# Kernel optimization log

Measured on AMD Instinct MI355X. Metric: run time of the kernel, lower is better.

## Reference

```python
import jax, jax.numpy as jnp
import numpy as np

B, T = 32, 1000
NN, NB, CTX = 512, 16, 64
EMB = 256
DCAT = 3 * EMB
H, L = 256, 4
PN, PB = 512, 2
S, V = 8, 64


def setup_inputs() -> dict:
    key = jax.random.key(0)
    ks = jax.random.split(key, 20)
    r = lambda i, shape, sc=1.0: jax.random.normal(ks[i], shape, dtype=jnp.float32) * sc
    nu_log = jnp.log(-jnp.log(jax.random.uniform(ks[8], (L, H), minval=0.5, maxval=0.95)))
    inp = {
        'neural_input': r(0, (B, T, NN)),
        'behavior_input': r(1, (B, T, NB)),
        'session_id': jax.random.randint(ks[2], (B,), 0, V),
        'subject_id': jax.random.randint(ks[3], (B,), 0, S),
        'session_table': r(4, (V, CTX), 0.02),
        'neural_W': r(5, (S, EMB, NN), 1.0 / np.sqrt(NN)),
        'neural_b': jnp.zeros((S, EMB), jnp.float32),
        'behavior_W': r(6, (S, EMB, NB), 1.0 / np.sqrt(NB)),
        'behavior_b': jnp.zeros((S, EMB), jnp.float32),
        'ctx_W': r(7, (EMB, CTX), 1.0 / np.sqrt(CTX)),
        'ctx_b': jnp.zeros((EMB,), jnp.float32),
        'nu_log': nu_log,
        'theta_log': jnp.log(jax.random.uniform(ks[9], (L, H), minval=1e-4, maxval=6.283)),
        'gamma_log': 0.5 * jnp.log1p(-jnp.exp(-2.0 * jnp.exp(nu_log))),
        'B_re': r(10, (L, H, DCAT), 1.0 / np.sqrt(2 * DCAT)),
        'B_im': r(11, (L, H, DCAT), 1.0 / np.sqrt(2 * DCAT)),
        'C_re': r(12, (L, DCAT, H), 1.0 / np.sqrt(H)),
        'C_im': r(13, (L, DCAT, H), 1.0 / np.sqrt(H)),
        'D_skip': r(14, (L, DCAT)),
        'dec_n_W': r(15, (S, PN, DCAT), 1.0 / np.sqrt(DCAT)),
        'dec_n_b': jnp.zeros((S, PN), jnp.float32),
        'dec_b_W': r(16, (S, PB, DCAT), 1.0 / np.sqrt(DCAT)),
        'dec_b_b': jnp.zeros((S, PB), jnp.float32),
    }
    return inp


def _lru(u, nu_log, theta_log, gamma_log, B_re, B_im, C_re, C_im, D_skip):
    # Linear Recurrent Unit: complex diagonal recurrence x_t = lam*x_{t-1} + gamma*B u_t
    lam = jnp.exp(-jnp.exp(nu_log) + 1j * jnp.exp(theta_log))  # [H]
    g = jnp.exp(gamma_log)[:, None]
    Bu = (jnp.einsum('bti,hi->bth', u, B_re * g)
          + 1j * jnp.einsum('bti,hi->bth', u, B_im * g))  # [B,T,H] complex

    def step(x, bu_t):
        x = lam * x + bu_t
        return x, x

    x0 = jnp.zeros((u.shape[0], nu_log.shape[0]), jnp.complex64)
    _, xs = jax.lax.scan(step, x0, jnp.swapaxes(Bu, 0, 1))
    xs = jnp.swapaxes(xs, 0, 1)  # [B,T,H]
    y = jnp.einsum('bth,oh->bto', xs, C_re + 1j * C_im).real + D_skip * u
    return y


def _forward(neural_input, behavior_input, session_table, neural_W, neural_b,
             behavior_W, behavior_b, ctx_W, ctx_b, nu_log, theta_log, gamma_log,
             B_re, B_im, C_re, C_im, D_skip, dec_n_W, dec_n_b, dec_b_W, dec_b_b,
             session_id, subject_id):
    act = jax.nn.relu
    Bsz, Ts, _ = neural_input.shape
    # session-token embedding -> context embedder (Linear is per-timestep, so embed once then broadcast)
    ctx = act(session_table[session_id] @ ctx_W.T + ctx_b)  # [B,EMB]
    ctx = jnp.broadcast_to(ctx[:, None, :], (Bsz, Ts, ctx.shape[-1]))
    # subject-routed embedders: gather per-sample weights, one batched GEMM
    en = act(jnp.einsum('btf,bef->bte', neural_input, neural_W[subject_id])
             + neural_b[subject_id][:, None, :])
    eb = act(jnp.einsum('btf,bef->bte', behavior_input, behavior_W[subject_id])
             + behavior_b[subject_id][:, None, :])
    h = jnp.concatenate([en, eb, ctx], axis=-1)  # [B,T,3*EMB]
    for l in range(nu_log.shape[0]):
        h = _lru(h, nu_log[l], theta_log[l], gamma_log[l],
                 B_re[l], B_im[l], C_re[l], C_im[l], D_skip[l])
    # subject-routed decoders
    pred_n = jax.nn.softplus(jnp.einsum('btd,bod->bto', h, dec_n_W[subject_id])
                             + dec_n_b[subject_id][:, None, :])
    pred_b = (jnp.einsum('btd,bod->bto', h, dec_b_W[subject_id])
              + dec_b_b[subject_id][:, None, :])
    return pred_n, pred_b


def reference(neural_input, behavior_input, session_id, subject_id, session_table,
              neural_W, neural_b, behavior_W, behavior_b, ctx_W, ctx_b,
              nu_log, theta_log, gamma_log, B_re, B_im, C_re, C_im, D_skip,
              dec_n_W, dec_n_b, dec_b_W, dec_b_b):
    return _forward(neural_input, behavior_input, session_table, neural_W, neural_b,
                    behavior_W, behavior_b, ctx_W, ctx_b, nu_log, theta_log, gamma_log,
                    B_re, B_im, C_re, C_im, D_skip, dec_n_W, dec_n_b, dec_b_W, dec_b_b,
                    session_id, subject_id)
```

## Files before the change

kernel.cpp:

```cpp
#include <hip/hip_runtime.h>

typedef __bf16 bf16;
typedef __bf16 bf16x8 __attribute__((ext_vector_type(8)));
typedef float f32x4 __attribute__((ext_vector_type(4)));

#define AS1 __attribute__((address_space(1)))
#define AS3 __attribute__((address_space(3)))

__device__ __forceinline__ void gll16(const void* g, void* l) {
    __builtin_amdgcn_global_load_lds((const AS1 void*)g, (AS3 void*)l, 16, 0, 0);
}

template<int EPI>
__device__ __forceinline__
void gemm_body(const bf16* __restrict__ Abase, long long aBstride, int lda,
               const bf16* __restrict__ Wbase, long long wSstride,
               const float* __restrict__ biasBase, int biasStride,
               void* __restrict__ Cbase, long long cBstride, int ldc,
               const float* __restrict__ dskip,
               const bf16* __restrict__ Ubase, long long uBstride,
               const int* __restrict__ subj,
               int M, int K, int nbn, char* smem)
{
    const int tid = threadIdx.x;
    const int lane = tid & 63;
    const int wid = tid >> 6;
    const int wm = wid >> 1, wn = wid & 1;
    const int l15 = lane & 15, lhi = lane >> 4;
    const int sw7 = l15 & 7;

    const int nwg = gridDim.x;
    const int bid = blockIdx.x;
    const int q = nwg >> 3, r = nwg & 7;
    const int xcd = bid & 7;
    const int sw = xcd * q + (xcd < r ? xcd : r) + (bid >> 3);
    const int m0 = (sw / nbn) * 256;
    const int n0 = (sw % nbn) * 128;

    const int b = blockIdx.z;
    const int s = subj ? subj[b] : 0;
    const bf16* A = Abase + (size_t)b * aBstride;
    const bf16* W = Wbase + (size_t)s * wSstride;
    const float* bias = biasBase ? biasBase + (size_t)s * biasStride : nullptr;
    const bf16* U = Ubase ? Ubase + (size_t)b * uBstride : nullptr;
    const size_t coff = (size_t)b * cBstride;
    const int Mc = M - 1;

    f32x4 acc[4][4];
    #pragma unroll
    for (int i = 0; i < 4; ++i)
        #pragma unroll
        for (int j = 0; j < 4; ++j)
            acc[i][j] = f32x4{0.f, 0.f, 0.f, 0.f};

    int rA[4], rB[4];
    #pragma unroll
    for (int f = 0; f < 4; ++f) {
        rA[f] = (wm*64 + f*16 + l15) * 128;
        rB[f] = (wn*64 + f*16 + l15) * 128;
    }

    const int sub  = tid >> 3;
    const int slot = tid & 7;
    const int ldsw = (wid << 10);

    auto stage = [&](int kt, int bufo) {
        #pragma unroll
        for (int c = 0; c < 4; ++c) {
            const int row = c*64 + sub;
            const int gk = (kt << 6) + ((slot ^ (row & 7)) << 3);
            int ar = m0 + row; if (ar > Mc) ar = Mc;
            gll16(A + (size_t)ar * lda + gk, smem + bufo + c*8192 + ldsw);
        }
        #pragma unroll
        for (int c = 0; c < 2; ++c) {
            const int row = c*64 + sub;
            const int gk = (kt << 6) + ((slot ^ (row & 7)) << 3);
            gll16(W + (size_t)(n0 + row) * K + gk, smem + bufo + 32768 + c*8192 + ldsw);
        }
    };

    const int nkt = K >> 6;
    stage(0, 0);
    if (nkt > 1) stage(1, 49152);
    asm volatile("s_waitcnt vmcnt(6)" ::: "memory");
    __builtin_amdgcn_s_barrier();

    int curo = 0, nno = 98304;
    for (int t = 0; t < nkt; ++t) {
        if (t + 2 < nkt) stage(t + 2, nno);

        const char* cb = smem + curo;
        #pragma unroll
        for (int kk = 0; kk < 2; ++kk) {
            const int so_ = (((kk << 2) | lhi) ^ sw7) << 4;
            bf16x8 af[4], bg[4];
            #pragma unroll
            for (int f = 0; f < 4; ++f) af[f] = *(const bf16x8*)(cb + rA[f] + so_);
            #pragma unroll
            for (int g = 0; g < 4; ++g) bg[g] = *(const bf16x8*)(cb + 32768 + rB[g] + so_);
            #pragma unroll
            for (int i = 0; i < 4; ++i)
                #pragma unroll
                for (int j = 0; j < 4; ++j)
                    acc[i][j] = __builtin_amdgcn_mfma_f32_16x16x32_bf16(
                        af[i], bg[j], acc[i][j], 0, 0, 0);
        }

        if (t + 2 < nkt) {
            asm volatile("s_waitcnt vmcnt(6)" ::: "memory");
        } else if (t + 1 < nkt) {
            asm volatile("s_waitcnt vmcnt(0)" ::: "memory");
        }
        if (t + 1 < nkt) __builtin_amdgcn_s_barrier();

        curo = (curo == 98304) ? 0 : curo + 49152;
        nno  = (nno  == 98304) ? 0 : nno  + 49152;
    }

    __syncthreads();
    #pragma unroll
    for (int i = 0; i < 4; ++i) {
        #pragma unroll
        for (int j = 0; j < 4; ++j) {
            const int colb = (wn*64 + j*16 + l15) * 2;
            const f32x4 v = acc[i][j];
            #pragma unroll
            for (int qq = 0; qq < 4; ++qq) {
                const int row = wm*64 + i*16 + lhi*4 + qq;
                const int ad = row*256 + (colb & 15) + ((((colb >> 4) ^ (row & 7)) & 15) << 4);
                *(bf16*)(smem + ad) = (bf16)v[qq];
            }
        }
    }
    __syncthreads();

    #pragma unroll
    for (int u = 0; u < 8; ++u) {
        const int chunk = u*512 + tid;
        const int rr = chunk >> 4, ss = chunk & 15;
        const int gr = m0 + rr;
        if (gr >= M) continue;
        const int col = n0 + ss*8;
        const bf16x8 v = *(const bf16x8*)(smem + rr*256 + ((ss ^ (rr & 7)) << 4));
        if constexpr (EPI == 0) {
            const size_t ci = coff + (size_t)gr * ldc + col;
            *(bf16x8*)((bf16*)Cbase + ci) = v;
        } else if constexpr (EPI == 1) {
            const float4 b0 = *(const float4*)(bias + col);
            const float4 b1 = *(const float4*)(bias + col + 4);
            bf16x8 o;
            o[0] = (bf16)fmaxf((float)v[0] + b0.x, 0.f);
            o[1] = (bf16)fmaxf((float)v[1] + b0.y, 0.f);
            o[2] = (bf16)fmaxf((float)v[2] + b0.z, 0.f);
            o[3] = (bf16)fmaxf((float)v[3] + b0.w, 0.f);
            o[4] = (bf16)fmaxf((float)v[4] + b1.x, 0.f);
            o[5] = (bf16)fmaxf((float)v[5] + b1.y, 0.f);
            o[6] = (bf16)fmaxf((float)v[6] + b1.z, 0.f);
            o[7] = (bf16)fmaxf((float)v[7] + b1.w, 0.f);
            const size_t ci = coff + (size_t)gr * ldc + col;
            *(bf16x8*)((bf16*)Cbase + ci) = o;
        } else if constexpr (EPI == 2) {
            const bf16x8 uv = *(const bf16x8*)(U + (size_t)gr * ldc + col);
            const float4 d0 = *(const float4*)(dskip + col);
            const float4 d1 = *(const float4*)(dskip + col + 4);
            bf16x8 o;
            o[0] = (bf16)((float)v[0] + d0.x * (float)uv[0]);
            o[1] = (bf16)((float)v[1] + d0.y * (float)uv[1]);
            o[2] = (bf16)((float)v[2] + d0.z * (float)uv[2]);
            o[3] = (bf16)((float)v[3] + d0.w * (float)uv[3]);
            o[4] = (bf16)((float)v[4] + d1.x * (float)uv[4]);
            o[5] = (bf16)((float)v[5] + d1.y * (float)uv[5]);
            o[6] = (bf16)((float)v[6] + d1.z * (float)uv[6]);
            o[7] = (bf16)((float)v[7] + d1.w * (float)uv[7]);
            const size_t ci = coff + (size_t)gr * ldc + col;
            *(bf16x8*)((bf16*)Cbase + ci) = o;
        } else {
            const float4 b0 = *(const float4*)(bias + col);
            const float4 b1 = *(const float4*)(bias + col + 4);
            float xv[8];
            xv[0] = (float)v[0] + b0.x; xv[1] = (float)v[1] + b0.y;
            xv[2] = (float)v[2] + b0.z; xv[3] = (float)v[3] + b0.w;
            xv[4] = (float)v[4] + b1.x; xv[5] = (float)v[5] + b1.y;
            xv[6] = (float)v[6] + b1.z; xv[7] = (float)v[7] + b1.w;
            float4 o0, o1;
            #pragma unroll
            for (int e = 0; e < 8; ++e) {
                const float x = xv[e];
                const float sp = fmaxf(x, 0.f) + log1pf(expf(-fabsf(x)));
                if (e < 4) ((float*)&o0)[e] = sp; else ((float*)&o1)[e-4] = sp;
            }
            const size_t ci = coff + (size_t)gr * ldc + col;
            *(float4*)((float*)Cbase + ci) = o0;
            *(float4*)((float*)Cbase + ci + 4) = o1;
        }
    }
}

#define GEMM_WRAP(NAME, EPI)                                                     \
__global__ __launch_bounds__(512, 2)                                             \
void NAME(const bf16* __restrict__ Abase, long long aBstride, int lda,           \
          const bf16* __restrict__ Wbase, long long wSstride,                    \
          const float* __restrict__ biasBase, int biasStride,                    \
          void* __restrict__ Cbase, long long cBstride, int ldc,                 \
          const float* __restrict__ dskip,                                       \
          const bf16* __restrict__ Ubase, long long uBstride,                    \
          const int* __restrict__ subj, int M, int K, int nbn)                   \
{                                                                                \
    __shared__ char smem[147456];                                                \
    gemm_body<EPI>(Abase, aBstride, lda, Wbase, wSstride, biasBase, biasStride,  \
                   Cbase, cBstride, ldc, dskip, Ubase, uBstride, subj,           \
                   M, K, nbn, smem);                                             \
}
GEMM_WRAP(gemm_en,  1)
GEMM_WRAP(gemm_bu,  0)
GEMM_WRAP(gemm_y,   2)
GEMM_WRAP(gemm_dec, 3)

__global__ void scan_finals(const bf16* __restrict__ Bu,
                            const float* __restrict__ nu_log,
                            const float* __restrict__ theta_log,
                            float2* __restrict__ finals)
{
    const int g = blockIdx.x * 256 + threadIdx.x;
    const int h = g & 255;
    const int c = (g >> 8) % 40;
    const int b = g / 10240;
    const float a  = expf(nu_log[h]);
    const float th = expf(theta_log[h]);
    const float mag = expf(-a);
    const float lre = mag * cosf(th), lim = mag * sinf(th);
    float xre = 0.f, xim = 0.f;
    const bf16* p = Bu + ((size_t)(b*1000 + c*25)) * 512 + h;
    for (int i = 0; i < 25; ++i) {
        const float bre = (float)p[0], bim = (float)p[256];
        const float nre = lre*xre - lim*xim + bre;
        const float nim = lre*xim + lim*xre + bim;
        xre = nre; xim = nim;
        p += 512;
    }
    finals[(b*40 + c)*256 + h] = make_float2(xre, xim);
}

__global__ void scan_carry(const float2* __restrict__ finals,
                           float2* __restrict__ carry,
                           const float* __restrict__ nu_log,
                           const float* __restrict__ theta_log)
{
    const int g = blockIdx.x * 256 + threadIdx.x;
    const int h = g & 255;
    const int b = g >> 8;
    const float a  = expf(nu_log[h]);
    const float th = expf(theta_log[h]);
    const float mag = expf(-25.f * a);
    const float ang = 25.f * th;
    const float cre = mag * cosf(ang), cim = mag * sinf(ang);
    float pre = 0.f, pim = 0.f;
    for (int c = 0; c < 40; ++c) {
        const int idx = (b*40 + c)*256 + h;
        carry[idx] = make_float2(pre, pim);
        const float2 f = finals[idx];
        const float nre = f.x + cre*pre - cim*pim;
        const float nim = f.y + cre*pim + cim*pre;
        pre = nre; pim = nim;
    }
}

__global__ void scan_emit(const bf16* __restrict__ Bu,
                          const float2* __restrict__ carry,
                          const float* __restrict__ nu_log,
                          const float* __restrict__ theta_log,
                          bf16* __restrict__ xs)
{
    const int g = blockIdx.x * 256 + threadIdx.x;
    const int h = g & 255;
    const int c = (g >> 8) % 40;
    const int b = g / 10240;
    const float a  = expf(nu_log[h]);
    const float th = expf(theta_log[h]);
    const float mag = expf(-a);
    const float lre = mag * cosf(th), lim = mag * sinf(th);
    const float2 cr = carry[(b*40 + c)*256 + h];
    float xre = cr.x, xim = cr.y;
    const bf16* p = Bu + ((size_t)(b*1000 + c*25)) * 512 + h;
    bf16* qp = xs + ((size_t)(b*1000 + c*25)) * 512 + h;
    for (int i = 0; i < 25; ++i) {
        const float bre = (float)p[0], bim = (float)p[256];
        const float nre = lre*xre - lim*xim + bre;
        const float nim = lre*xim + lim*xre + bim;
        xre = nre; xim = nim;
        qp[0] = (bf16)xre; qp[256] = (bf16)xim;
        p += 512; qp += 512;
    }
}

__global__ void cast8_kern(const float* __restrict__ src, bf16* __restrict__ dst, int n8)
{
    const int i = blockIdx.x * 256 + threadIdx.x;
    if (i >= n8) return;
    const float4* s = (const float4*)src + (size_t)i*2;
    const float4 v0 = s[0], v1 = s[1];
    bf16x8 o;
    o[0] = (bf16)v0.x; o[1] = (bf16)v0.y; o[2] = (bf16)v0.z; o[3] = (bf16)v0.w;
    o[4] = (bf16)v1.x; o[5] = (bf16)v1.y; o[6] = (bf16)v1.z; o[7] = (bf16)v1.w;
    *((bf16x8*)dst + i) = o;
}

__global__ void packWB_kern(const float* __restrict__ Bre, const float* __restrict__ Bim,
                            const float* __restrict__ glog, bf16* __restrict__ WB)
{
    const int idx = blockIdx.x * 256 + threadIdx.x;
    if (idx >= 4*512*768) return;
    const int l = idx / (512*768);
    const int r = idx - l*(512*768);
    const int n = r / 768;
    const int k = r - n*768;
    float v;
    if (n < 256) v = Bre[((size_t)(l*256 + n))*768 + k] * expf(glog[l*256 + n]);
    else         v = Bim[((size_t)(l*256 + (n-256)))*768 + k] * expf(glog[l*256 + (n-256)]);
    WB[idx] = (bf16)v;
}

__global__ void packWC_kern(const float* __restrict__ Cre, const float* __restrict__ Cim,
                            bf16* __restrict__ WC)
{
    const int idx = blockIdx.x * 256 + threadIdx.x;
    if (idx >= 4*768*512) return;
    const int l = idx / (768*512);
    const int r = idx - l*(768*512);
    const int o = r / 512;
    const int k = r - o*512;
    const float v = (k < 256) ? Cre[((size_t)(l*768 + o))*256 + k]
                              : -Cim[((size_t)(l*768 + o))*256 + (k - 256)];
    WC[idx] = (bf16)v;
}

__global__ void ctx_kern(const float* __restrict__ st, const int* __restrict__ sess,
                         const float* __restrict__ cW, const float* __restrict__ cb,
                         float* __restrict__ ctx)
{
    const int b = blockIdx.x;
    const int e = threadIdx.x;
    const int sid = sess[b];
    const float* r = st + (size_t)sid * 64;
    const float* w = cW + (size_t)e * 64;
    float acc = cb[e];
    #pragma unroll 8
    for (int i = 0; i < 64; ++i) acc += r[i] * w[i];
    ctx[b*256 + e] = fmaxf(acc, 0.f);
}

__global__ void ebctx_kern(const float* __restrict__ behav,
                           const float* __restrict__ bW,
                           const float* __restrict__ bB,
                           const int* __restrict__ subj,
                           const float* __restrict__ ctx,
                           bf16* __restrict__ h0)
{
    const int b  = blockIdx.x >> 3;
    const int tc = blockIdx.x & 7;
    const int e = threadIdx.x;
    const int s = subj[b];
    float wreg[16];
    const float* w = bW + ((size_t)(s*256) + e)*16;
    #pragma unroll
    for (int i = 0; i < 16; ++i) wreg[i] = w[i];
    const float bb_ = bB[s*256 + e];
    const bf16 cx = (bf16)ctx[b*256 + e];
    const int t0 = tc * 125;
    for (int t = t0; t < t0 + 125; ++t) {
        const int blk = b*1000 + t;
        const float* bi = behav + (size_t)blk * 16;
        float acc = bb_;
        #pragma unroll
        for (int i = 0; i < 16; ++i) acc += bi[i] * wreg[i];
        bf16* hp = h0 + (size_t)blk * 768;
        hp[256 + e] = (bf16)fmaxf(acc, 0.f);
        hp[512 + e] = cx;
    }
}

__global__ void predb_kern(const bf16* __restrict__ h, const float* __restrict__ W,
                           const float* __restrict__ bb, const int* __restrict__ subj,
                           float* __restrict__ out)
{
    const int lane = threadIdx.x & 63;
    const int wid  = threadIdx.x >> 6;
    const int row  = blockIdx.x * 4 + wid;
    const int b = row / 1000;
    const int s = subj[b];
    const bf16* hr = h + (size_t)row * 768;
    const float* w0 = W + (size_t)(s*2) * 768;
    const float* w1 = w0 + 768;
    float a0 = 0.f, a1 = 0.f;
    #pragma unroll
    for (int j = 0; j < 12; ++j) {
        const int idx = j*64 + lane;
        const float hv = (float)hr[idx];
        a0 += hv * w0[idx];
        a1 += hv * w1[idx];
    }
    #pragma unroll
    for (int m = 32; m >= 1; m >>= 1) {
        a0 += __shfl_xor(a0, m);
        a1 += __shfl_xor(a1, m);
    }
    if (lane == 0) {
        out[(size_t)row*2 + 0] = a0 + bb[s*2 + 0];
        out[(size_t)row*2 + 1] = a1 + bb[s*2 + 1];
    }
}

extern "C" void kernel_launch(void* const* d_in, const int* in_sizes, int n_in,
                              void* d_out, int out_size, void* d_ws, size_t ws_size,
                              hipStream_t stream)
{
    const float* neural_input   = (const float*)d_in[0];
    const float* behavior_input = (const float*)d_in[1];
    const int*   session_id     = (const int*)d_in[2];
    const int*   subject_id     = (const int*)d_in[3];
    const float* session_table  = (const float*)d_in[4];
    const float* neural_W  = (const float*)d_in[5];
    const float* neural_b  = (const float*)d_in[6];
    const float* behavior_W = (const float*)d_in[7];
    const float* behavior_b = (const float*)d_in[8];
    const float* ctx_W = (const float*)d_in[9];
    const float* ctx_b = (const float*)d_in[10];
    const float* nu_log    = (const float*)d_in[11];
    const float* theta_log = (const float*)d_in[12];
    const float* gamma_log = (const float*)d_in[13];
    const float* B_re = (const float*)d_in[14];
    const float* B_im = (const float*)d_in[15];
    const float* C_re = (const float*)d_in[16];
    const float* C_im = (const float*)d_in[17];
    const float* D_skip = (const float*)d_in[18];
    const float* dec_n_W = (const float*)d_in[19];
    const float* dec_n_b = (const float*)d_in[20];
    const float* dec_b_W = (const float*)d_in[21];
    const float* dec_b_b = (const float*)d_in[22];
    float* out = (float*)d_out;

    char* ws = (char*)d_ws;
    size_t off = 0;
    auto alloc = [&](size_t bytes) -> char* {
        char* p = ws + off;
        off += (bytes + 255) & ~(size_t)255;
        return p;
    };
    bf16*   Wn      = (bf16*)alloc((size_t)8*256*512*2);
    bf16*   Wd      = (bf16*)alloc((size_t)8*512*768*2);
    bf16*   WB      = (bf16*)alloc((size_t)4*512*768*2);
    bf16*   WC      = (bf16*)alloc((size_t)4*768*512*2);
    float*  ctxbuf  = (float*)alloc((size_t)32*256*4);
    bf16*   hA      = (bf16*)alloc((size_t)32*1000*768*2);
    bf16*   hB      = (bf16*)alloc((size_t)32*1000*768*2);
    bf16*   xs      = (bf16*)alloc((size_t)32*1000*512*2);
    float2* finals  = (float2*)alloc((size_t)32*40*256*8);
    float2* carry   = (float2*)alloc((size_t)32*40*256*8);
    bf16*   Bu      = (bf16*)alloc((size_t)32*1000*512*2);
    bf16*   nbf     = Bu;

    cast8_kern<<<dim3(512),   256, 0, stream>>>(neural_W, Wn, 131072);
    cast8_kern<<<dim3(1536),  256, 0, stream>>>(dec_n_W,  Wd, 393216);
    packWB_kern<<<dim3(6144), 256, 0, stream>>>(B_re, B_im, gamma_log, WB);
    packWC_kern<<<dim3(6144), 256, 0, stream>>>(C_re, C_im, WC);
    ctx_kern<<<dim3(32), 256, 0, stream>>>(session_table, session_id, ctx_W, ctx_b, ctxbuf);
    cast8_kern<<<dim3(8000), 256, 0, stream>>>(neural_input, nbf, 2048000);

    ebctx_kern<<<dim3(256), 256, 0, stream>>>(behavior_input, behavior_W, behavior_b,
                                              subject_id, ctxbuf, hA);
    gemm_en<<<dim3(8, 1, 32), 512, 0, stream>>>(
        nbf, 512000LL, 512, Wn, 131072LL, neural_b, 256,
        hA, 768000LL, 768, nullptr, nullptr, 0LL, subject_id, 1000, 512, 2);

    for (int l = 0; l < 4; ++l) {
        const bf16* hin  = (l & 1) ? hB : hA;
        bf16*       hout = (l & 1) ? hA : hB;
        gemm_bu<<<dim3(500, 1, 1), 512, 0, stream>>>(
            hin, 0LL, 768, WB + (size_t)l*393216, 0LL, nullptr, 0,
            Bu, 0LL, 512, nullptr, nullptr, 0LL, nullptr, 32000, 768, 4);
        scan_finals<<<dim3(1280), 256, 0, stream>>>(Bu, nu_log + l*256, theta_log + l*256, finals);
        scan_carry<<<dim3(32), 256, 0, stream>>>(finals, carry, nu_log + l*256, theta_log + l*256);
        scan_emit<<<dim3(1280), 256, 0, stream>>>(Bu, carry, nu_log + l*256, theta_log + l*256, xs);
        gemm_y<<<dim3(750, 1, 1), 512, 0, stream>>>(
            xs, 0LL, 512, WC + (size_t)l*393216, 0LL, nullptr, 0,
            hout, 0LL, 768, D_skip + l*768, hin, 0LL, nullptr, 32000, 512, 6);
    }

    gemm_dec<<<dim3(16, 1, 32), 512, 0, stream>>>(
        hA, 768000LL, 768, Wd, 393216LL, dec_n_b, 512,
        out, 512000LL, 512, nullptr, nullptr, 0LL, subject_id, 1000, 768, 4);
    predb_kern<<<dim3(8000), 256, 0, stream>>>(hA, dec_b_W, dec_b_b, subject_id,
                                               out + 16384000);
}
```

Baseline: 610.6 us.

## Add register-staged GEMM loads, vectorize scan kernels, use fast softplus intrinsics

Adds a template option so the Bu and Y GEMMs stage tiles through registers (global load into registers, then a swizzled LDS store) instead of direct global-to-LDS loads, overlapping the next load with the MFMA loop. The scan kernels now have each thread process two adjacent hidden channels using bf16x2 loads and stores and float4 carry access, with half the blocks. The decoder softplus switches to __expf/__logf. These are separate ideas that trade register pressure, parallelism and accuracy for fewer memory transactions and cheaper math.

Result: slower. 920.9 us (+50.8%).

```diff
diff --git a/kernel.cpp b/kernel.cpp
--- a/kernel.cpp
+++ b/kernel.cpp
@@ -1,6 +1,7 @@
 #include <hip/hip_runtime.h>
 
 typedef __bf16 bf16;
+typedef __bf16 bf16x2 __attribute__((ext_vector_type(2)));
 typedef __bf16 bf16x8 __attribute__((ext_vector_type(8)));
 typedef float f32x4 __attribute__((ext_vector_type(4)));
 
@@ -11,7 +12,7 @@
     __builtin_amdgcn_global_load_lds((const AS1 void*)g, (AS3 void*)l, 16, 0, 0);
 }
 
-template<int EPI>
+template<int EPI, int STAGE>
 __device__ __forceinline__
 void gemm_body(const bf16* __restrict__ Abase, long long aBstride, int lda,
                const bf16* __restrict__ Wbase, long long wSstride,
@@ -64,7 +65,7 @@
     const int slot = tid & 7;
     const int ldsw = (wid << 10);
 
-    auto stage = [&](int kt, int bufo) {
+    auto stage_lds = [&](int kt, int bufo) {
         #pragma unroll
         for (int c = 0; c < 4; ++c) {
             const int row = c*64 + sub;
@@ -80,15 +81,47 @@
         }
     };
 
+    float4 rgA[4], rgB[2];
+    auto loadreg = [&](int kt) {
+        #pragma unroll
+        for (int c = 0; c < 4; ++c) {
+            const int row = c*64 + sub;
+            int ar = m0 + row; if (ar > Mc) ar = Mc;
+            rgA[c] = *(const float4*)(A + (size_t)ar * lda + (kt << 6) + (slot << 3));
+        }
+        #pragma unroll
+        for (int c = 0; c < 2; ++c)
+            rgB[c] = *(const float4*)(W + (size_t)(n0 + c*64 + sub) * K + (kt << 6) + (slot << 3));
+    };
+    auto writereg = [&](int bufo) {
+        const int wsl = sub*128 + ((slot ^ (sub & 7)) << 4);
+        #pragma unroll
+        for (int c = 0; c < 4; ++c)
+            *(float4*)(smem + bufo + c*8192 + wsl) = rgA[c];
+        #pragma unroll
+        for (int c = 0; c < 2; ++c)
+            *(float4*)(smem + bufo + 32768 + c*8192 + wsl) = rgB[c];
+    };
+
     const int nkt = K >> 6;
-    stage(0, 0);
-    if (nkt > 1) stage(1, 49152);
-    asm volatile("s_waitcnt vmcnt(6)" ::: "memory");
-    __builtin_amdgcn_s_barrier();
+    if constexpr (STAGE == 0) {
+        stage_lds(0, 0);
+        if (nkt > 1) stage_lds(1, 49152);
+        asm volatile("s_waitcnt vmcnt(6)" ::: "memory");
+        __builtin_amdgcn_s_barrier();
+    } else {
+        loadreg(0); writereg(0);
+        loadreg(1); writereg(49152);
+        __syncthreads();
+    }
 
     int curo = 0, nno = 98304;
     for (int t = 0; t < nkt; ++t) {
-        if (t + 2 < nkt) stage(t + 2, nno);
+        if constexpr (STAGE == 0) {
+            if (t + 2 < nkt) stage_lds(t + 2, nno);
+        } else {
+            if (t + 2 < nkt) loadreg(t + 2);
+        }
 
         const char* cb = smem + curo;
         #pragma unroll
@@ -107,12 +140,17 @@
                         af[i], bg[j], acc[i][j], 0, 0, 0);
         }
 
-        if (t + 2 < nkt) {
-            asm volatile("s_waitcnt vmcnt(6)" ::: "memory");
-        } else if (t + 1 < nkt) {
-            asm volatile("s_waitcnt vmcnt(0)" ::: "memory");
-        }
-        if (t + 1 < nkt) __builtin_amdgcn_s_barrier();
+        if constexpr (STAGE == 0) {
+            if (t + 2 < nkt) {
+                asm volatile("s_waitcnt vmcnt(6)" ::: "memory");
+            } else if (t + 1 < nkt) {
+                asm volatile("s_waitcnt vmcnt(0)" ::: "memory");
+            }
+            if (t + 1 < nkt) __builtin_amdgcn_s_barrier();
+        } else {
+            if (t + 2 < nkt) writereg(nno);
+            if (t + 1 < nkt) __syncthreads();
+        }
 
         curo = (curo == 98304) ? 0 : curo + 49152;
         nno  = (nno  == 98304) ? 0 : nno  + 49152;
@@ -187,7 +225,7 @@
             #pragma unroll
             for (int e = 0; e < 8; ++e) {
                 const float x = xv[e];
-                const float sp = fmaxf(x, 0.f) + log1pf(expf(-fabsf(x)));
+                const float sp = fmaxf(x, 0.f) + __logf(1.f + __expf(-fabsf(x)));
                 if (e < 4) ((float*)&o0)[e] = sp; else ((float*)&o1)[e-4] = sp;
             }
             const size_t ci = coff + (size_t)gr * ldc + col;
@@ -197,7 +235,7 @@
     }
 }
 
-#define GEMM_WRAP(NAME, EPI)                                                     \
+#define GEMM_WRAP(NAME, EPI, STAGE)                                              \
 __global__ __launch_bounds__(512, 2)                                             \
 void NAME(const bf16* __restrict__ Abase, long long aBstride, int lda,           \
           const bf16* __restrict__ Wbase, long long wSstride,                    \
@@ -208,14 +246,14 @@
           const int* __restrict__ subj, int M, int K, int nbn)                   \
 {                                                                                \
     __shared__ char smem[147456];                                                \
-    gemm_body<EPI>(Abase, aBstride, lda, Wbase, wSstride, biasBase, biasStride,  \
-                   Cbase, cBstride, ldc, dskip, Ubase, uBstride, subj,           \
-                   M, K, nbn, smem);                                             \
-}
-GEMM_WRAP(gemm_en,  1)
-GEMM_WRAP(gemm_bu,  0)
-GEMM_WRAP(gemm_y,   2)
-GEMM_WRAP(gemm_dec, 3)
+    gemm_body<EPI, STAGE>(Abase, aBstride, lda, Wbase, wSstride, biasBase,       \
+                   biasStride, Cbase, cBstride, ldc, dskip, Ubase, uBstride,     \
+                   subj, M, K, nbn, smem);                                       \
+}
+GEMM_WRAP(gemm_en,  1, 0)
+GEMM_WRAP(gemm_bu,  0, 1)
+GEMM_WRAP(gemm_y,   2, 1)
+GEMM_WRAP(gemm_dec, 3, 0)
 
 __global__ void scan_finals(const bf16* __restrict__ Bu,
                             const float* __restrict__ nu_log,
@@ -223,23 +261,30 @@
                             float2* __restrict__ finals)
 {
     const int g = blockIdx.x * 256 + threadIdx.x;
-    const int h = g & 255;
-    const int c = (g >> 8) % 40;
-    const int b = g / 10240;
-    const float a  = expf(nu_log[h]);
-    const float th = expf(theta_log[h]);
-    const float mag = expf(-a);
-    const float lre = mag * cosf(th), lim = mag * sinf(th);
-    float xre = 0.f, xim = 0.f;
-    const bf16* p = Bu + ((size_t)(b*1000 + c*25)) * 512 + h;
+    const int hp = g & 127;
+    const int c = (g >> 7) % 40;
+    const int b = g / 5120;
+    const int h0 = hp * 2;
+    const float a0 = expf(nu_log[h0]),   t0 = expf(theta_log[h0]);
+    const float a1 = expf(nu_log[h0+1]), t1 = expf(theta_log[h0+1]);
+    const float m0_ = expf(-a0), m1_ = expf(-a1);
+    const float lre0 = m0_*cosf(t0), lim0 = m0_*sinf(t0);
+    const float lre1 = m1_*cosf(t1), lim1 = m1_*sinf(t1);
+    float xr0 = 0.f, xi0 = 0.f, xr1 = 0.f, xi1 = 0.f;
+    const bf16* p = Bu + ((size_t)(b*1000 + c*25)) * 512 + h0;
     for (int i = 0; i < 25; ++i) {
-        const float bre = (float)p[0], bim = (float)p[256];
-        const float nre = lre*xre - lim*xim + bre;
-        const float nim = lre*xim + lim*xre + bim;
-        xre = nre; xim = nim;
+        const bf16x2 re = *(const bf16x2*)(p);
+        const bf16x2 im = *(const bf16x2*)(p + 256);
+        float nr = lre0*xr0 - lim0*xi0 + (float)re[0];
+        float ni = lre0*xi0 + lim0*xr0 + (float)im[0];
+        xr0 = nr; xi0 = ni;
+        nr = lre1*xr1 - lim1*xi1 + (float)re[1];
+        ni = lre1*xi1 + lim1*xr1 + (float)im[1];
+        xr1 = nr; xi1 = ni;
         p += 512;
     }
-    finals[(b*40 + c)*256 + h] = make_float2(xre, xim);
+    float4* fo = (float4*)&finals[(b*40 + c)*256 + h0];
+    *fo = make_float4(xr0, xi0, xr1, xi1);
 }
 
 __global__ void scan_carry(const float2* __restrict__ finals,
@@ -273,23 +318,33 @@
                           bf16* __restrict__ xs)
 {
     const int g = blockIdx.x * 256 + threadIdx.x;
-    const int h = g & 255;
-    const int c = (g >> 8) % 40;
-    const int b = g / 10240;
-    const float a  = expf(nu_log[h]);
-    const float th = expf(theta_log[h]);
-    const float mag = expf(-a);
-    const float lre = mag * cosf(th), lim = mag * sinf(th);
-    const float2 cr = carry[(b*40 + c)*256 + h];
-    float xre = cr.x, xim = cr.y;
-    const bf16* p = Bu + ((size_t)(b*1000 + c*25)) * 512 + h;
-    bf16* qp = xs + ((size_t)(b*1000 + c*25)) * 512 + h;
+    const int hp = g & 127;
+    const int c = (g >> 7) % 40;
+    const int b = g / 5120;
+    const int h0 = hp * 2;
+    const float a0 = expf(nu_log[h0]),   t0 = expf(theta_log[h0]);
+    const float a1 = expf(nu_log[h0+1]), t1 = expf(theta_log[h0+1]);
+    const float m0_ = expf(-a0), m1_ = expf(-a1);
+    const float lre0 = m0_*cosf(t0), lim0 = m0_*sinf(t0);
+    const float lre1 = m1_*cosf(t1), lim1 = m1_*sinf(t1);
+    const float4 cr = *(const float4*)&carry[(b*40 + c)*256 + h0];
+    float xr0 = cr.x, xi0 = cr.y, xr1 = cr.z, xi1 = cr.w;
+    const bf16* p = Bu + ((size_t)(b*1000 + c*25)) * 512 + h0;
+    bf16* qp = xs + ((size_t)(b*1000 + c*25)) * 512 + h0;
     for (int i = 0; i < 25; ++i) {
-        const float bre = (float)p[0], bim = (float)p[256];
-        const float nre = lre*xre - lim*xim + bre;
-        const float nim = lre*xim + lim*xre + bim;
-        xre = nre; xim = nim;
-        qp[0] = (bf16)xre; qp[256] = (bf16)xim;
+        const bf16x2 re = *(const bf16x2*)(p);
+        const bf16x2 im = *(const bf16x2*)(p + 256);
+        float nr = lre0*xr0 - lim0*xi0 + (float)re[0];
+        float ni = lre0*xi0 + lim0*xr0 + (float)im[0];
+        xr0 = nr; xi0 = ni;
+        nr = lre1*xr1 - lim1*xi1 + (float)re[1];
+        ni = lre1*xi1 + lim1*xr1 + (float)im[1];
+        xr1 = nr; xi1 = ni;
+        bf16x2 ro, io;
+        ro[0] = (bf16)xr0; ro[1] = (bf16)xr1;
+        io[0] = (bf16)xi0; io[1] = (bf16)xi1;
+        *(bf16x2*)(qp) = ro;
+        *(bf16x2*)(qp + 256) = io;
         p += 512; qp += 512;
     }
 }
@@ -479,9 +534,9 @@
         gemm_bu<<<dim3(500, 1, 1), 512, 0, stream>>>(
             hin, 0LL, 768, WB + (size_t)l*393216, 0LL, nullptr, 0,
             Bu, 0LL, 512, nullptr, nullptr, 0LL, nullptr, 32000, 768, 4);
-        scan_finals<<<dim3(1280), 256, 0, stream>>>(Bu, nu_log + l*256, theta_log + l*256, finals);
+        scan_finals<<<dim3(640), 256, 0, stream>>>(Bu, nu_log + l*256, theta_log + l*256, finals);
         scan_carry<<<dim3(32), 256, 0, stream>>>(finals, carry, nu_log + l*256, theta_log + l*256);
-        scan_emit<<<dim3(1280), 256, 0, stream>>>(Bu, carry, nu_log + l*256, theta_log + l*256, xs);
+        scan_emit<<<dim3(640), 256, 0, stream>>>(Bu, carry, nu_log + l*256, theta_log + l*256, xs);
         gemm_y<<<dim3(750, 1, 1), 512, 0, stream>>>(
             xs, 0LL, 512, WC + (size_t)l*393216, 0LL, nullptr, 0,
             hout, 0LL, 768, D_skip + l*768, hin, 0LL, nullptr, 32000, 512, 6);
```
